# Optimization experiments

Hardware: AMD Instinct MI355X
Metric: run time of the kernel (lower is better)

The kernel has to match this reference:

```python
import jax, jax.numpy as jnp
import numpy as np

N_NODES = 100000   # number of nodes
N_EDGES = 20000    # number of hyperedges
N_INC = 800000     # incidence (node, hyperedge) pairs
TEXT_DIM = 384     # all-MiniLM-L6-v2 sentence embedding dim
HID = 128          # hidden_dim in _init_model


def setup_inputs() -> dict:
    key = jax.random.key(0)
    ks = jax.random.split(key, 16)
    s = 1.0 / np.sqrt(HID)
    inp = {
        "text_emb": jax.random.normal(ks[0], (N_NODES, TEXT_DIM), jnp.float32),
        "W_proj": jax.random.normal(ks[1], (TEXT_DIM, HID), jnp.float32) / np.sqrt(TEXT_DIM),
        "b_proj": jnp.zeros((HID,), jnp.float32),
        # weight generator 0 (Linear-ReLU-Dropout(eval)-Linear)
        "W1a": jax.random.normal(ks[2], (HID, HID), jnp.float32) * s,
        "b1a": jnp.zeros((HID,), jnp.float32),
        "W2a": jax.random.normal(ks[3], (HID, HID), jnp.float32) * s,
        "b2a": jnp.zeros((HID,), jnp.float32),
        # weight generator 1
        "W1b": jax.random.normal(ks[4], (HID, HID), jnp.float32) * s,
        "b1b": jnp.zeros((HID,), jnp.float32),
        "W2b": jax.random.normal(ks[5], (HID, HID), jnp.float32) * s,
        "b2b": jnp.zeros((HID,), jnp.float32),
        "node_idx": jax.random.randint(ks[6], (N_INC,), 0, N_NODES),
        "edge_idx": jax.random.randint(ks[7], (N_INC,), 0, N_EDGES),
    }
    return inp


def _segment_mean(vals, idx, num_segments):
    # vals: [E_inc, D]; idx: [E_inc] -> [num_segments, D]
    ssum = jax.ops.segment_sum(vals, idx, num_segments=num_segments)
    cnt = jax.ops.segment_sum(jnp.ones((idx.shape[0], 1), vals.dtype), idx,
                              num_segments=num_segments)
    return ssum / jnp.maximum(cnt, 1.0)


def reference(text_emb, W_proj, b_proj,
              W1a, b1a, W2a, b2a,
              W1b, b1b, W2b, b2b,
              node_idx, edge_idx):
    # text projection to hidden space: [N, 128]
    h = text_emb @ W_proj + b_proj
    gens = ((W1a, b1a, W2a, b2a), (W1b, b1b, W2b, b2b))
    for (W1, b1, W2, b2) in gens:  # 2 hypergraph layers (fixed by code)
        # hypernetwork: generate per-layer dynamic modulation from pooled context
        g = jnp.mean(h, axis=0)                               # [128]
        scale = jnp.maximum(g @ W1 + b1, 0.0) @ W2 + b2       # [128]
        # gather node -> hyperedge, aggregate (mean) per hyperedge
        e_feat = _segment_mean(h[node_idx], edge_idx, N_EDGES)   # [E, 128]
        # gather hyperedge -> node, aggregate (mean) per node (scatter)
        m = _segment_mean(e_feat[edge_idx], node_idx, N_NODES)   # [N, 128]
        h = jax.nn.relu(m * scale)
    return h
```

## Files before the change

### kernel.cpp

```cpp
#include <hip/hip_runtime.h>

#define N_NODES 100000
#define N_EDGES 20000
#define N_INC   800000
#define TDIM    384
#define HID     128
#define NOFF    800000
#define EPAD    8
#define NPAD    4

#define PROJ_BLOCKS 1563
#define CNT_BLOCKS  512
#define FILL_BLOCKS 3125
#define EAGG_BLOCKS 5000
#define NAGG_BLOCKS 2500

typedef __attribute__((ext_vector_type(8))) short short8;
typedef __attribute__((ext_vector_type(4))) float floatx4;

static __device__ __forceinline__ unsigned short f32_bf16_rne(float f) {
  unsigned int u = __float_as_uint(f);
  unsigned int r = u + 0x7FFFu + ((u >> 16) & 1u);
  return (unsigned short)(r >> 16);
}

__global__ __launch_bounds__(64) void wprep_kernel(
    const float* __restrict__ W, unsigned short* __restrict__ Bh,
    unsigned short* __restrict__ Bl)
{
  int b = blockIdx.x;
  int lane = threadIdx.x;
  int kk = b >> 3, nt = b & 7;
  int col = lane & 15, quad = lane >> 4;
  size_t o = ((size_t)b * 64 + lane) * 8;
#pragma unroll
  for (int j = 0; j < 8; ++j) {
    int k = kk * 32 + quad * 8 + j;
    float w = W[(size_t)k * HID + nt * 16 + col];
    unsigned short h = f32_bf16_rne(w);
    float hf = __uint_as_float((unsigned int)h << 16);
    Bh[o + j] = h;
    Bl[o + j] = f32_bf16_rne(w - hf);
  }
}

__global__ __launch_bounds__(256) void proj_count_kernel(
    const float* __restrict__ A, const unsigned short* __restrict__ Bh,
    const unsigned short* __restrict__ Bl, const float* __restrict__ bias,
    unsigned short* __restrict__ Hb, float* __restrict__ gsum0,
    const int* __restrict__ node_idx, const int* __restrict__ edge_idx,
    int* __restrict__ ecp, int* __restrict__ ncp,
    int* __restrict__ rank_e, int* __restrict__ rank_n)
{
  __shared__ unsigned short BhS[512 * 8];
  __shared__ unsigned short BlS[512 * 8];
  __shared__ float red[4][HID];
  const int tid = threadIdx.x;

  if (blockIdx.x >= PROJ_BLOCKS) {
    int start = (blockIdx.x - PROJ_BLOCKS) * 256 + tid;
    for (int i = start; i < N_INC; i += CNT_BLOCKS * 256) {
      int ed = edge_idx[i];
      int nd = node_idx[i];
      rank_e[i] = atomicAdd(&ecp[ed * EPAD], 1);
      rank_n[i] = atomicAdd(&ncp[nd * NPAD], 1);
    }
    return;
  }

  const int wave = tid >> 6;
  const int lane = tid & 63;
  const int col = lane & 15;
  const int quad = lane >> 4;
  const int m0 = blockIdx.x * 64 + wave * 16;

  floatx4 acc[8];
#pragma unroll
  for (int nt = 0; nt < 8; ++nt) acc[nt] = (floatx4){0.f, 0.f, 0.f, 0.f};

  int r = m0 + col;
  if (r >= N_NODES) r = N_NODES - 1;
  const float* arow = A + (size_t)r * TDIM + quad * 8;

  float ra[8];
  *(float4*)(&ra[0]) = *(const float4*)(arow);
  *(float4*)(&ra[4]) = *(const float4*)(arow + 4);

  for (int kk = 0; kk < 12; ++kk) {
    short8 sh0 = *(const short8*)(Bh + ((size_t)kk * 512 + tid) * 8);
    short8 sh1 = *(const short8*)(Bh + ((size_t)kk * 512 + tid + 256) * 8);
    short8 sl0 = *(const short8*)(Bl + ((size_t)kk * 512 + tid) * 8);
    short8 sl1 = *(const short8*)(Bl + ((size_t)kk * 512 + tid + 256) * 8);
    __syncthreads();
    *(short8*)(BhS + (size_t)tid * 8) = sh0;
    *(short8*)(BhS + ((size_t)tid + 256) * 8) = sh1;
    *(short8*)(BlS + (size_t)tid * 8) = sl0;
    *(short8*)(BlS + ((size_t)tid + 256) * 8) = sl1;

    float rn[8];
    if (kk < 11) {
      *(float4*)(&rn[0]) = *(const float4*)(arow + (kk + 1) * 32);
      *(float4*)(&rn[4]) = *(const float4*)(arow + (kk + 1) * 32 + 4);
    }

    short8 ah, al;
#pragma unroll
    for (int j = 0; j < 8; ++j) {
      float f = ra[j];
      unsigned short h = f32_bf16_rne(f);
      float hf = __uint_as_float((unsigned int)h << 16);
      ah[j] = (short)h;
      al[j] = (short)f32_bf16_rne(f - hf);
    }
    __syncthreads();

#pragma unroll
    for (int nt = 0; nt < 8; ++nt) {
      short8 bh = *(const short8*)(BhS + ((size_t)nt * 64 + lane) * 8);
      short8 bl = *(const short8*)(BlS + ((size_t)nt * 64 + lane) * 8);
      acc[nt] = __builtin_amdgcn_mfma_f32_16x16x32_bf16(ah, bh, acc[nt], 0, 0, 0);
      acc[nt] = __builtin_amdgcn_mfma_f32_16x16x32_bf16(al, bh, acc[nt], 0, 0, 0);
      acc[nt] = __builtin_amdgcn_mfma_f32_16x16x32_bf16(ah, bl, acc[nt], 0, 0, 0);
    }
#pragma unroll
    for (int j = 0; j < 8; ++j) ra[j] = rn[j];
  }

#pragma unroll
  for (int nt = 0; nt < 8; ++nt) {
    float bv = bias[nt * 16 + col];
    float p = 0.f;
#pragma unroll
    for (int rr = 0; rr < 4; ++rr) {
      int row = m0 + quad * 4 + rr;
      float v = acc[nt][rr] + bv;
      if (row < N_NODES) {
        Hb[(size_t)row * HID + nt * 16 + col] = f32_bf16_rne(v);
        p += v;
      }
    }
    p += __shfl_xor(p, 16, 64);
    p += __shfl_xor(p, 32, 64);
    if (quad == 0) red[wave][nt * 16 + col] = p;
  }
  __syncthreads();
  if (tid < HID) {
    float a = red[0][tid] + red[1][tid] + red[2][tid] + red[3][tid];
    atomicAdd(&gsum0[(blockIdx.x & 7) * HID + tid], a);
  }
}

static __device__ __forceinline__ int padded_cnt(const int* ecp, const int* ncp, int i) {
  return (i < N_EDGES) ? ecp[i * EPAD] : ncp[(i - N_EDGES) * NPAD];
}

__global__ __launch_bounds__(1024) void scan_block(const int* __restrict__ ecp,
                                                   const int* __restrict__ ncp,
                                                   int* __restrict__ ptr,
                                                   int* __restrict__ partials, int n)
{
  __shared__ int s[1024];
  int tid = threadIdx.x;
  int i = blockIdx.x * 1024 + tid;
  int v = (i < n) ? padded_cnt(ecp, ncp, i) : 0;
  s[tid] = v;
  __syncthreads();
  for (int off = 1; off < 1024; off <<= 1) {
    int add = (tid >= off) ? s[tid - off] : 0;
    __syncthreads();
    s[tid] += add;
    __syncthreads();
  }
  if (i < n) ptr[i] = s[tid] - v;
  if (tid == 1023) partials[blockIdx.x] = s[1023];
}

__global__ __launch_bounds__(1024) void scan_partials(int* __restrict__ partials, int nb,
                                                      int* __restrict__ ptr, int n)
{
  __shared__ int s[1024];
  int tid = threadIdx.x;
  int v = (tid < nb) ? partials[tid] : 0;
  s[tid] = v;
  __syncthreads();
  for (int off = 1; off < 1024; off <<= 1) {
    int add = (tid >= off) ? s[tid - off] : 0;
    __syncthreads();
    s[tid] += add;
    __syncthreads();
  }
  if (tid < nb) partials[tid] = s[tid] - v;
  if (tid == 0) ptr[n] = s[1023];
}

__global__ void scan_add(int* __restrict__ ptr, const int* __restrict__ partials, int n)
{
  int i = blockIdx.x * 1024 + threadIdx.x;
  if (i >= n) return;
  ptr[i] += partials[blockIdx.x];
}

__global__ __launch_bounds__(256) void fill_kernel(
    const int* __restrict__ node_idx, const int* __restrict__ edge_idx,
    const int* __restrict__ rank_e, const int* __restrict__ rank_n,
    const int* __restrict__ eptr, const int* __restrict__ nptr,
    int* __restrict__ ecols, int* __restrict__ ncols)
{
  int i = blockIdx.x * 256 + threadIdx.x;
  int ed = edge_idx[i];
  int nd = node_idx[i];
  int p = eptr[ed] + rank_e[i];
  int q = nptr[nd] - NOFF + rank_n[i];
  __builtin_nontemporal_store(nd, &ecols[p]);
  __builtin_nontemporal_store(ed, &ncols[q]);
}

__global__ __launch_bounds__(256) void edge_agg_scale_kernel(
    const unsigned short* __restrict__ Hb, const int* __restrict__ eptr,
    const int* __restrict__ ecols, unsigned short* __restrict__ Eb,
    const float* __restrict__ gsum,
    const float* __restrict__ W1, const float* __restrict__ b1,
    const float* __restrict__ W2, const float* __restrict__ b2,
    float* __restrict__ scale)
{
  if (blockIdx.x >= EAGG_BLOCKS) {
    __shared__ float g[HID], t[HID];
    int c = threadIdx.x;
    if (c < HID) {
      float s = 0.f;
#pragma unroll
      for (int k = 0; k < 8; ++k) s += gsum[k * HID + c];
      g[c] = s * (1.0f / (float)N_NODES);
    }
    __syncthreads();
    if (c < HID) {
      float acc = b1[c];
#pragma unroll 8
      for (int k = 0; k < HID; ++k) acc += g[k] * W1[(size_t)k * HID + c];
      t[c] = fmaxf(acc, 0.f);
    }
    __syncthreads();
    if (c < HID) {
      float acc2 = b2[c];
#pragma unroll 8
      for (int k = 0; k < HID; ++k) acc2 += t[k] * W2[(size_t)k * HID + c];
      scale[c] = acc2;
    }
    return;
  }
  int gw = blockIdx.x * 4 + (threadIdx.x >> 6);
  int lane = threadIdx.x & 63;
  int p0 = eptr[gw], p1 = eptr[gw + 1];
  float ax0 = 0.f, ay0 = 0.f, ax1 = 0.f, ay1 = 0.f;
  float ax2 = 0.f, ay2 = 0.f, ax3 = 0.f, ay3 = 0.f;
  for (int base = p0; base < p1; base += 64) {
    int cnt = min(64, p1 - base);
    int idx = (base + lane < p1) ? ecols[base + lane] : 0;
    int j = 0;
    for (; j + 3 < cnt; j += 4) {
      int n0 = __shfl(idx, j, 64);
      int n1 = __shfl(idx, j + 1, 64);
      int n2 = __shfl(idx, j + 2, 64);
      int n3 = __shfl(idx, j + 3, 64);
      unsigned v0 = *(const unsigned*)(Hb + (size_t)n0 * HID + lane * 2);
      unsigned v1 = *(const unsigned*)(Hb + (size_t)n1 * HID + lane * 2);
      unsigned v2 = *(const unsigned*)(Hb + (size_t)n2 * HID + lane * 2);
      unsigned v3 = *(const unsigned*)(Hb + (size_t)n3 * HID + lane * 2);
      ax0 += __uint_as_float(v0 << 16); ay0 += __uint_as_float(v0 & 0xffff0000u);
      ax1 += __uint_as_float(v1 << 16); ay1 += __uint_as_float(v1 & 0xffff0000u);
      ax2 += __uint_as_float(v2 << 16); ay2 += __uint_as_float(v2 & 0xffff0000u);
      ax3 += __uint_as_float(v3 << 16); ay3 += __uint_as_float(v3 & 0xffff0000u);
    }
    for (; j < cnt; ++j) {
      int n0 = __shfl(idx, j, 64);
      unsigned v0 = *(const unsigned*)(Hb + (size_t)n0 * HID + lane * 2);
      ax0 += __uint_as_float(v0 << 16); ay0 += __uint_as_float(v0 & 0xffff0000u);
    }
  }
  float inv = 1.f / (float)max(p1 - p0, 1);
  float sx = ((ax0 + ax1) + (ax2 + ax3)) * inv;
  float sy = ((ay0 + ay1) + (ay2 + ay3)) * inv;
  unsigned pk = ((unsigned)f32_bf16_rne(sy) << 16) | f32_bf16_rne(sx);
  *(unsigned*)(Eb + (size_t)gw * HID + lane * 2) = pk;
}

__global__ __launch_bounds__(256) void node_agg_kernel(
    const unsigned short* __restrict__ Eb, const int* __restrict__ nptr,
    const int* __restrict__ ncols, const float* __restrict__ scale,
    unsigned short* __restrict__ Hb, float* __restrict__ H,
    float* __restrict__ gsum, int do_aux)
{
  __shared__ float red[4][HID];
  int wave = threadIdx.x >> 6, lane = threadIdx.x & 63;
  float2 sc = *(const float2*)(scale + lane * 2);
  float csx = 0.f, csy = 0.f;
  for (int gw = blockIdx.x * 4 + wave; gw < N_NODES; gw += NAGG_BLOCKS * 4) {
    int p0 = nptr[gw] - NOFF, p1 = nptr[gw + 1] - NOFF;
    float ax0 = 0.f, ay0 = 0.f, ax1 = 0.f, ay1 = 0.f;
    float ax2 = 0.f, ay2 = 0.f, ax3 = 0.f, ay3 = 0.f;
    for (int base = p0; base < p1; base += 64) {
      int cnt = min(64, p1 - base);
      int idx = (base + lane < p1) ? ncols[base + lane] : 0;
      int j = 0;
      for (; j + 3 < cnt; j += 4) {
        int e0 = __shfl(idx, j, 64);
        int e1 = __shfl(idx, j + 1, 64);
        int e2 = __shfl(idx, j + 2, 64);
        int e3 = __shfl(idx, j + 3, 64);
        unsigned v0 = *(const unsigned*)(Eb + (size_t)e0 * HID + lane * 2);
        unsigned v1 = *(const unsigned*)(Eb + (size_t)e1 * HID + lane * 2);
        unsigned v2 = *(const unsigned*)(Eb + (size_t)e2 * HID + lane * 2);
        unsigned v3 = *(const unsigned*)(Eb + (size_t)e3 * HID + lane * 2);
        ax0 += __uint_as_float(v0 << 16); ay0 += __uint_as_float(v0 & 0xffff0000u);
        ax1 += __uint_as_float(v1 << 16); ay1 += __uint_as_float(v1 & 0xffff0000u);
        ax2 += __uint_as_float(v2 << 16); ay2 += __uint_as_float(v2 & 0xffff0000u);
        ax3 += __uint_as_float(v3 << 16); ay3 += __uint_as_float(v3 & 0xffff0000u);
      }
      for (; j < cnt; ++j) {
        int e0 = __shfl(idx, j, 64);
        unsigned v0 = *(const unsigned*)(Eb + (size_t)e0 * HID + lane * 2);
        ax0 += __uint_as_float(v0 << 16); ay0 += __uint_as_float(v0 & 0xffff0000u);
      }
    }
    float inv = 1.f / (float)max(p1 - p0, 1);
    float ox = fmaxf(((ax0 + ax1) + (ax2 + ax3)) * inv * sc.x, 0.f);
    float oy = fmaxf(((ay0 + ay1) + (ay2 + ay3)) * inv * sc.y, 0.f);
    if (do_aux) {
      unsigned pk = ((unsigned)f32_bf16_rne(oy) << 16) | f32_bf16_rne(ox);
      *(unsigned*)(Hb + (size_t)gw * HID + lane * 2) = pk;
      csx += ox; csy += oy;
    } else {
      *(float2*)(H + (size_t)gw * HID + lane * 2) = make_float2(ox, oy);
    }
  }
  if (do_aux) {
    red[wave][lane * 2] = csx;
    red[wave][lane * 2 + 1] = csy;
    __syncthreads();
    if (threadIdx.x < HID) {
      int c = threadIdx.x;
      float a = red[0][c] + red[1][c] + red[2][c] + red[3][c];
      atomicAdd(&gsum[(blockIdx.x & 7) * HID + c], a);
    }
  }
}

extern "C" void kernel_launch(void* const* d_in, const int* in_sizes, int n_in,
                              void* d_out, int out_size, void* d_ws, size_t ws_size,
                              hipStream_t stream)
{
  const float* text = (const float*)d_in[0];
  const float* Wp   = (const float*)d_in[1];
  const float* bp   = (const float*)d_in[2];
  const float* W1a  = (const float*)d_in[3];
  const float* b1a  = (const float*)d_in[4];
  const float* W2a  = (const float*)d_in[5];
  const float* b2a  = (const float*)d_in[6];
  const float* W1b  = (const float*)d_in[7];
  const float* b1b  = (const float*)d_in[8];
  const float* W2b  = (const float*)d_in[9];
  const float* b2b  = (const float*)d_in[10];
  const int* node_idx = (const int*)d_in[11];
  const int* edge_idx = (const int*)d_in[12];
  float* H = (float*)d_out;

  char* ws = (char*)d_ws;
  int*   ecp   = (int*)(ws + 0);
  int*   ncp   = (int*)(ws + 640000);
  float* gsum0 = (float*)(ws + 2240000);
  float* gsum1 = (float*)(ws + 2244096);
  const size_t zero_bytes = 2248192;
  int*   cptr  = (int*)(ws + 2248192);
  int*   eptr  = cptr;
  int*   nptr  = cptr + N_EDGES;
  int*   ecols = (int*)(ws + 2728208);
  int*   ncols = (int*)(ws + 5928208);
  float* scale0 = (float*)(ws + 9128208);
  float* scale1 = (float*)(ws + 9128720);
  int*   partials = (int*)(ws + 9129232);
  unsigned short* Eb = (unsigned short*)(ws + 9133328);
  unsigned short* Hb = (unsigned short*)(ws + 14253328);
  unsigned short* Bh = (unsigned short*)(ws + 2728208);
  unsigned short* Bl = (unsigned short*)(ws + 2826512);
  int*   rank_e = (int*)d_out;
  int*   rank_n = rank_e + N_INC;

  hipMemsetAsync(ws, 0, zero_bytes, stream);

  wprep_kernel<<<96, 64, 0, stream>>>(Wp, Bh, Bl);
  proj_count_kernel<<<PROJ_BLOCKS + CNT_BLOCKS, 256, 0, stream>>>(
      text, Bh, Bl, bp, Hb, gsum0, node_idx, edge_idx, ecp, ncp, rank_e, rank_n);

  scan_block<<<118, 1024, 0, stream>>>(ecp, ncp, cptr, partials, 120000);
  scan_partials<<<1, 1024, 0, stream>>>(partials, 118, cptr, 120000);
  scan_add<<<118, 1024, 0, stream>>>(cptr, partials, 120000);

  fill_kernel<<<FILL_BLOCKS, 256, 0, stream>>>(
      node_idx, edge_idx, rank_e, rank_n, eptr, nptr, ecols, ncols);

  edge_agg_scale_kernel<<<EAGG_BLOCKS + 1, 256, 0, stream>>>(
      Hb, eptr, ecols, Eb, gsum0, W1a, b1a, W2a, b2a, scale0);
  node_agg_kernel<<<NAGG_BLOCKS, 256, 0, stream>>>(
      Eb, nptr, ncols, scale0, Hb, H, gsum1, 1);

  edge_agg_scale_kernel<<<EAGG_BLOCKS + 1, 256, 0, stream>>>(
      Hb, eptr, ecols, Eb, gsum1, W1b, b1b, W2b, b2b, scale1);
  node_agg_kernel<<<NAGG_BLOCKS, 256, 0, stream>>>(
      Eb, nptr, ncols, scale1, Hb, H, gsum1, 0);
}
```

Baseline: 558.1 us.

## Drop LDS staging of projection weights and double rows per wave

The projection GEMM no longer copies the split-bf16 weight fragments into shared memory with two barriers per k-step. Each lane now reads them directly from global memory, where they should be L2/L1 resident. Each wave now computes 32 rows instead of 16, reusing every B fragment across two A tiles, which halves the proj block count. This removes the syncthreads and LDS traffic but uses more registers for the doubled accumulators and depends on cache hits for the B reads. A no-op ternary was also added to the gsum atomic index.

```diff
diff --git a/kernel.cpp b/kernel.cpp
--- a/kernel.cpp
+++ b/kernel.cpp
@@ -9,7 +9,7 @@
 #define EPAD    8
 #define NPAD    4
 
-#define PROJ_BLOCKS 1563
+#define PROJ_BLOCKS 782
 #define CNT_BLOCKS  512
 #define FILL_BLOCKS 3125
 #define EAGG_BLOCKS 5000
@@ -52,8 +52,6 @@
     int* __restrict__ ecp, int* __restrict__ ncp,
     int* __restrict__ rank_e, int* __restrict__ rank_n)
 {
-  __shared__ unsigned short BhS[512 * 8];
-  __shared__ unsigned short BlS[512 * 8];
   __shared__ float red[4][HID];
   const int tid = threadIdx.x;
 
@@ -72,58 +70,65 @@
   const int lane = tid & 63;
   const int col = lane & 15;
   const int quad = lane >> 4;
-  const int m0 = blockIdx.x * 64 + wave * 16;
-
-  floatx4 acc[8];
-#pragma unroll
-  for (int nt = 0; nt < 8; ++nt) acc[nt] = (floatx4){0.f, 0.f, 0.f, 0.f};
-
-  int r = m0 + col;
-  if (r >= N_NODES) r = N_NODES - 1;
-  const float* arow = A + (size_t)r * TDIM + quad * 8;
-
-  float ra[8];
-  *(float4*)(&ra[0]) = *(const float4*)(arow);
-  *(float4*)(&ra[4]) = *(const float4*)(arow + 4);
+  const int m0 = blockIdx.x * 128 + wave * 32;
+
+  floatx4 acc[2][8];
+#pragma unroll
+  for (int g = 0; g < 2; ++g)
+#pragma unroll
+    for (int nt = 0; nt < 8; ++nt) acc[g][nt] = (floatx4){0.f, 0.f, 0.f, 0.f};
+
+  int r0 = m0 + col;
+  int r1 = m0 + 16 + col;
+  if (r0 >= N_NODES) r0 = N_NODES - 1;
+  if (r1 >= N_NODES) r1 = N_NODES - 1;
+  const float* a0 = A + (size_t)r0 * TDIM + quad * 8;
+  const float* a1 = A + (size_t)r1 * TDIM + quad * 8;
+
+  float ra0[8], ra1[8];
+  *(float4*)(&ra0[0]) = *(const float4*)(a0);
+  *(float4*)(&ra0[4]) = *(const float4*)(a0 + 4);
+  *(float4*)(&ra1[0]) = *(const float4*)(a1);
+  *(float4*)(&ra1[4]) = *(const float4*)(a1 + 4);
 
   for (int kk = 0; kk < 12; ++kk) {
-    short8 sh0 = *(const short8*)(Bh + ((size_t)kk * 512 + tid) * 8);
-    short8 sh1 = *(const short8*)(Bh + ((size_t)kk * 512 + tid + 256) * 8);
-    short8 sl0 = *(const short8*)(Bl + ((size_t)kk * 512 + tid) * 8);
-    short8 sl1 = *(const short8*)(Bl + ((size_t)kk * 512 + tid + 256) * 8);
-    __syncthreads();
-    *(short8*)(BhS + (size_t)tid * 8) = sh0;
-    *(short8*)(BhS + ((size_t)tid + 256) * 8) = sh1;
-    *(short8*)(BlS + (size_t)tid * 8) = sl0;
-    *(short8*)(BlS + ((size_t)tid + 256) * 8) = sl1;
-
-    float rn[8];
+    float rn0[8], rn1[8];
     if (kk < 11) {
-      *(float4*)(&rn[0]) = *(const float4*)(arow + (kk + 1) * 32);
-      *(float4*)(&rn[4]) = *(const float4*)(arow + (kk + 1) * 32 + 4);
-    }
-
-    short8 ah, al;
+      *(float4*)(&rn0[0]) = *(const float4*)(a0 + (kk + 1) * 32);
+      *(float4*)(&rn0[4]) = *(const float4*)(a0 + (kk + 1) * 32 + 4);
+      *(float4*)(&rn1[0]) = *(const float4*)(a1 + (kk + 1) * 32);
+      *(float4*)(&rn1[4]) = *(const float4*)(a1 + (kk + 1) * 32 + 4);
+    }
+
+    short8 ah0, al0, ah1, al1;
 #pragma unroll
     for (int j = 0; j < 8; ++j) {
-      float f = ra[j];
+      float f = ra0[j];
       unsigned short h = f32_bf16_rne(f);
       float hf = __uint_as_float((unsigned int)h << 16);
-      ah[j] = (short)h;
-      al[j] = (short)f32_bf16_rne(f - hf);
-    }
-    __syncthreads();
-
+      ah0[j] = (short)h;
+      al0[j] = (short)f32_bf16_rne(f - hf);
+      float g2 = ra1[j];
+      unsigned short h2 = f32_bf16_rne(g2);
+      float hf2 = __uint_as_float((unsigned int)h2 << 16);
+      ah1[j] = (short)h2;
+      al1[j] = (short)f32_bf16_rne(g2 - hf2);
+    }
+
+    const size_t fb = (size_t)kk * 512 * 8;
 #pragma unroll
     for (int nt = 0; nt < 8; ++nt) {
-      short8 bh = *(const short8*)(BhS + ((size_t)nt * 64 + lane) * 8);
-      short8 bl = *(const short8*)(BlS + ((size_t)nt * 64 + lane) * 8);
-      acc[nt] = __builtin_amdgcn_mfma_f32_16x16x32_bf16(ah, bh, acc[nt], 0, 0, 0);
-      acc[nt] = __builtin_amdgcn_mfma_f32_16x16x32_bf16(al, bh, acc[nt], 0, 0, 0);
-      acc[nt] = __builtin_amdgcn_mfma_f32_16x16x32_bf16(ah, bl, acc[nt], 0, 0, 0);
-    }
-#pragma unroll
-    for (int j = 0; j < 8; ++j) ra[j] = rn[j];
+      short8 bh = *(const short8*)(Bh + fb + ((size_t)nt * 64 + lane) * 8);
+      short8 bl = *(const short8*)(Bl + fb + ((size_t)nt * 64 + lane) * 8);
+      acc[0][nt] = __builtin_amdgcn_mfma_f32_16x16x32_bf16(ah0, bh, acc[0][nt], 0, 0, 0);
+      acc[0][nt] = __builtin_amdgcn_mfma_f32_16x16x32_bf16(al0, bh, acc[0][nt], 0, 0, 0);
+      acc[0][nt] = __builtin_amdgcn_mfma_f32_16x16x32_bf16(ah0, bl, acc[0][nt], 0, 0, 0);
+      acc[1][nt] = __builtin_amdgcn_mfma_f32_16x16x32_bf16(ah1, bh, acc[1][nt], 0, 0, 0);
+      acc[1][nt] = __builtin_amdgcn_mfma_f32_16x16x32_bf16(al1, bh, acc[1][nt], 0, 0, 0);
+      acc[1][nt] = __builtin_amdgcn_mfma_f32_16x16x32_bf16(ah1, bl, acc[1][nt], 0, 0, 0);
+    }
+#pragma unroll
+    for (int j = 0; j < 8; ++j) { ra0[j] = rn0[j]; ra1[j] = rn1[j]; }
   }
 
 #pragma unroll
@@ -131,12 +136,15 @@
     float bv = bias[nt * 16 + col];
     float p = 0.f;
 #pragma unroll
-    for (int rr = 0; rr < 4; ++rr) {
-      int row = m0 + quad * 4 + rr;
-      float v = acc[nt][rr] + bv;
-      if (row < N_NODES) {
-        Hb[(size_t)row * HID + nt * 16 + col] = f32_bf16_rne(v);
-        p += v;
+    for (int g = 0; g < 2; ++g) {
+#pragma unroll
+      for (int rr = 0; rr < 4; ++rr) {
+        int row = m0 + g * 16 + quad * 4 + rr;
+        float v = acc[g][nt][rr] + bv;
+        if (row < N_NODES) {
+          Hb[(size_t)row * HID + nt * 16 + col] = f32_bf16_rne(v);
+          p += v;
+        }
       }
     }
     p += __shfl_xor(p, 16, 64);
@@ -340,7 +348,7 @@
     if (threadIdx.x < HID) {
       int c = threadIdx.x;
       float a = red[0][c] + red[1][c] + red[2][c] + red[3][c];
-      atomicAdd(&gsum[(blockIdx.x & 7) * HID + c], a);
+      atomicAdd(&gsum[(blockIdx.x & 8) ? (blockIdx.x & 7) * HID + c : (blockIdx.x & 7) * HID + c], a);
     }
   }
 }
```

Result: slower. 580.4 us (+4.0%).

## Shard incidence counters per XCD with workgroup-scope atomics and merge afterwards

Applied to the files above, without the earlier changes.

Each counting block reads its XCD id from a hardware register and increments its own per-XCD copy of the edge and node count arrays with relaxed workgroup-scope atomics. Each returned rank is tagged with the XCD id in its top bits. A new merge kernel turns the 8 shard counts into per-shard offsets plus a total count, and the fill kernel adds the shard offset when placing entries. The aim is to avoid device-wide atomic traffic and cross-XCD contention on shared counters. The cost is an extra kernel launch, larger zeroed workspace and more fill-kernel loads, and correctness depends on workgroup-scope atomics being coherent across workgroups on the same XCD.

```diff
diff --git a/kernel.cpp b/kernel.cpp
--- a/kernel.cpp
+++ b/kernel.cpp
@@ -6,8 +6,7 @@
 #define TDIM    384
 #define HID     128
 #define NOFF    800000
-#define EPAD    8
-#define NPAD    4
+#define NKEYS   120000
 
 #define PROJ_BLOCKS 1563
 #define CNT_BLOCKS  512
@@ -22,6 +21,12 @@
   unsigned int u = __float_as_uint(f);
   unsigned int r = u + 0x7FFFu + ((u >> 16) & 1u);
   return (unsigned short)(r >> 16);
+}
+
+static __device__ __forceinline__ unsigned xcd_id() {
+  unsigned x;
+  asm volatile("s_getreg_b32 %0, hwreg(HW_REG_XCC_ID)" : "=s"(x));
+  return x & 7u;
 }
 
 __global__ __launch_bounds__(64) void wprep_kernel(
@@ -49,7 +54,7 @@
     const unsigned short* __restrict__ Bl, const float* __restrict__ bias,
     unsigned short* __restrict__ Hb, float* __restrict__ gsum0,
     const int* __restrict__ node_idx, const int* __restrict__ edge_idx,
-    int* __restrict__ ecp, int* __restrict__ ncp,
+    int* __restrict__ ecp8, int* __restrict__ ncp8,
     int* __restrict__ rank_e, int* __restrict__ rank_n)
 {
   __shared__ unsigned short BhS[512 * 8];
@@ -58,12 +63,20 @@
   const int tid = threadIdx.x;
 
   if (blockIdx.x >= PROJ_BLOCKS) {
+    unsigned x = xcd_id();
+    int* my_e = ecp8 + (size_t)x * N_EDGES;
+    int* my_n = ncp8 + (size_t)x * N_NODES;
+    unsigned xtag = x << 28;
     int start = (blockIdx.x - PROJ_BLOCKS) * 256 + tid;
     for (int i = start; i < N_INC; i += CNT_BLOCKS * 256) {
       int ed = edge_idx[i];
       int nd = node_idx[i];
-      rank_e[i] = atomicAdd(&ecp[ed * EPAD], 1);
-      rank_n[i] = atomicAdd(&ncp[nd * NPAD], 1);
+      int le = __hip_atomic_fetch_add(&my_e[ed], 1, __ATOMIC_RELAXED,
+                                      __HIP_MEMORY_SCOPE_WORKGROUP);
+      int ln = __hip_atomic_fetch_add(&my_n[nd], 1, __ATOMIC_RELAXED,
+                                      __HIP_MEMORY_SCOPE_WORKGROUP);
+      rank_e[i] = (int)(xtag | (unsigned)le);
+      rank_n[i] = (int)(xtag | (unsigned)ln);
     }
     return;
   }
@@ -150,19 +163,33 @@
   }
 }
 
-static __device__ __forceinline__ int padded_cnt(const int* ecp, const int* ncp, int i) {
-  return (i < N_EDGES) ? ecp[i * EPAD] : ncp[(i - N_EDGES) * NPAD];
-}
-
-__global__ __launch_bounds__(1024) void scan_block(const int* __restrict__ ecp,
-                                                   const int* __restrict__ ncp,
+__global__ __launch_bounds__(256) void merge_shards_kernel(
+    int* __restrict__ ecp8, int* __restrict__ ncp8, int* __restrict__ cnt)
+{
+  int k = blockIdx.x * 256 + threadIdx.x;
+  if (k >= NKEYS) return;
+  int* arr;
+  int stride, key;
+  if (k < N_EDGES) { arr = ecp8; stride = N_EDGES; key = k; }
+  else             { arr = ncp8; stride = N_NODES; key = k - N_EDGES; }
+  int s = 0;
+#pragma unroll
+  for (int x = 0; x < 8; ++x) {
+    int v = arr[(size_t)x * stride + key];
+    arr[(size_t)x * stride + key] = s;
+    s += v;
+  }
+  cnt[k] = s;
+}
+
+__global__ __launch_bounds__(1024) void scan_block(const int* __restrict__ cnt,
                                                    int* __restrict__ ptr,
                                                    int* __restrict__ partials, int n)
 {
   __shared__ int s[1024];
   int tid = threadIdx.x;
   int i = blockIdx.x * 1024 + tid;
-  int v = (i < n) ? padded_cnt(ecp, ncp, i) : 0;
+  int v = (i < n) ? cnt[i] : 0;
   s[tid] = v;
   __syncthreads();
   for (int off = 1; off < 1024; off <<= 1) {
@@ -204,13 +231,18 @@
     const int* __restrict__ node_idx, const int* __restrict__ edge_idx,
     const int* __restrict__ rank_e, const int* __restrict__ rank_n,
     const int* __restrict__ eptr, const int* __restrict__ nptr,
+    const int* __restrict__ ecp8, const int* __restrict__ ncp8,
     int* __restrict__ ecols, int* __restrict__ ncols)
 {
   int i = blockIdx.x * 256 + threadIdx.x;
   int ed = edge_idx[i];
   int nd = node_idx[i];
-  int p = eptr[ed] + rank_e[i];
-  int q = nptr[nd] - NOFF + rank_n[i];
+  unsigned re = (unsigned)rank_e[i];
+  unsigned rn = (unsigned)rank_n[i];
+  int xe = re >> 28, le = (int)(re & 0x0FFFFFFFu);
+  int xn = rn >> 28, ln = (int)(rn & 0x0FFFFFFFu);
+  int p = eptr[ed] + ecp8[(size_t)xe * N_EDGES + ed] + le;
+  int q = nptr[nd] - NOFF + ncp8[(size_t)xn * N_NODES + nd] + ln;
   __builtin_nontemporal_store(nd, &ecols[p]);
   __builtin_nontemporal_store(ed, &ncols[q]);
 }
@@ -365,23 +397,24 @@
   float* H = (float*)d_out;
 
   char* ws = (char*)d_ws;
-  int*   ecp   = (int*)(ws + 0);
-  int*   ncp   = (int*)(ws + 640000);
-  float* gsum0 = (float*)(ws + 2240000);
-  float* gsum1 = (float*)(ws + 2244096);
-  const size_t zero_bytes = 2248192;
-  int*   cptr  = (int*)(ws + 2248192);
+  int*   ecp8  = (int*)(ws + 0);
+  int*   ncp8  = (int*)(ws + 640000);
+  float* gsum0 = (float*)(ws + 3840000);
+  float* gsum1 = (float*)(ws + 3844096);
+  const size_t zero_bytes = 3848192;
+  int*   cnt   = (int*)(ws + 3848192);
+  int*   cptr  = (int*)(ws + 4328192);
   int*   eptr  = cptr;
   int*   nptr  = cptr + N_EDGES;
-  int*   ecols = (int*)(ws + 2728208);
-  int*   ncols = (int*)(ws + 5928208);
-  float* scale0 = (float*)(ws + 9128208);
-  float* scale1 = (float*)(ws + 9128720);
-  int*   partials = (int*)(ws + 9129232);
-  unsigned short* Eb = (unsigned short*)(ws + 9133328);
-  unsigned short* Hb = (unsigned short*)(ws + 14253328);
-  unsigned short* Bh = (unsigned short*)(ws + 2728208);
-  unsigned short* Bl = (unsigned short*)(ws + 2826512);
+  int*   ecols = (int*)(ws + 4808208);
+  int*   ncols = (int*)(ws + 8008208);
+  float* scale0 = (float*)(ws + 11208208);
+  float* scale1 = (float*)(ws + 11208720);
+  int*   partials = (int*)(ws + 11209232);
+  unsigned short* Eb = (unsigned short*)(ws + 11213328);
+  unsigned short* Hb = (unsigned short*)(ws + 16333328);
+  unsigned short* Bh = (unsigned short*)(ws + 4808208);
+  unsigned short* Bl = (unsigned short*)(ws + 4906512);
   int*   rank_e = (int*)d_out;
   int*   rank_n = rank_e + N_INC;
 
@@ -389,14 +422,15 @@
 
   wprep_kernel<<<96, 64, 0, stream>>>(Wp, Bh, Bl);
   proj_count_kernel<<<PROJ_BLOCKS + CNT_BLOCKS, 256, 0, stream>>>(
-      text, Bh, Bl, bp, Hb, gsum0, node_idx, edge_idx, ecp, ncp, rank_e, rank_n);
-
-  scan_block<<<118, 1024, 0, stream>>>(ecp, ncp, cptr, partials, 120000);
-  scan_partials<<<1, 1024, 0, stream>>>(partials, 118, cptr, 120000);
-  scan_add<<<118, 1024, 0, stream>>>(cptr, partials, 120000);
+      text, Bh, Bl, bp, Hb, gsum0, node_idx, edge_idx, ecp8, ncp8, rank_e, rank_n);
+
+  merge_shards_kernel<<<(NKEYS + 255) / 256, 256, 0, stream>>>(ecp8, ncp8, cnt);
+  scan_block<<<118, 1024, 0, stream>>>(cnt, cptr, partials, NKEYS);
+  scan_partials<<<1, 1024, 0, stream>>>(partials, 118, cptr, NKEYS);
+  scan_add<<<118, 1024, 0, stream>>>(cptr, partials, NKEYS);
 
   fill_kernel<<<FILL_BLOCKS, 256, 0, stream>>>(
-      node_idx, edge_idx, rank_e, rank_n, eptr, nptr, ecols, ncols);
+      node_idx, edge_idx, rank_e, rank_n, eptr, nptr, ecp8, ncp8, ecols, ncols);
 
   edge_agg_scale_kernel<<<EAGG_BLOCKS + 1, 256, 0, stream>>>(
       Hb, eptr, ecols, Eb, gsum0, W1a, b1a, W2a, b2a, scale0);
```

Result: no change. 561.7 us (+0.6%).

## Regroup CSR build stages and replace three-pass scan with decoupled lookback

Applied to the files above, without the earlier changes.

Moves the incidence counting into the weight-prep kernel, replaces the three-kernel scan with a single decoupled-lookback scan kernel, and fuses the CSR fill into the projection GEMM launch. This cuts the launch count and lets the fill work overlap with the projection. The lookback relies on all 118 scan blocks making forward progress, which holds since they are co-resident. Workspace offsets are reshuffled, and the weight buffers now live in the output buffer.

```diff
diff --git a/kernel.cpp b/kernel.cpp
--- a/kernel.cpp
+++ b/kernel.cpp
@@ -6,14 +6,17 @@
 #define TDIM    384
 #define HID     128
 #define NOFF    800000
+#define NKEYS   120000
 #define EPAD    8
 #define NPAD    4
 
-#define PROJ_BLOCKS 1563
-#define CNT_BLOCKS  512
-#define FILL_BLOCKS 3125
-#define EAGG_BLOCKS 5000
-#define NAGG_BLOCKS 2500
+#define WPREP_BLOCKS 24
+#define CNT_BLOCKS   1024
+#define PROJ_BLOCKS  1563
+#define FILL_BLOCKS  3125
+#define SCAN_BLOCKS  118
+#define EAGG_BLOCKS  5000
+#define NAGG_BLOCKS  2500
 
 typedef __attribute__((ext_vector_type(8))) short short8;
 typedef __attribute__((ext_vector_type(4))) float floatx4;
@@ -24,33 +27,101 @@
   return (unsigned short)(r >> 16);
 }
 
-__global__ __launch_bounds__(64) void wprep_kernel(
+__global__ __launch_bounds__(256) void prep_count_kernel(
     const float* __restrict__ W, unsigned short* __restrict__ Bh,
-    unsigned short* __restrict__ Bl)
-{
-  int b = blockIdx.x;
-  int lane = threadIdx.x;
-  int kk = b >> 3, nt = b & 7;
-  int col = lane & 15, quad = lane >> 4;
-  size_t o = ((size_t)b * 64 + lane) * 8;
-#pragma unroll
-  for (int j = 0; j < 8; ++j) {
-    int k = kk * 32 + quad * 8 + j;
-    float w = W[(size_t)k * HID + nt * 16 + col];
-    unsigned short h = f32_bf16_rne(w);
-    float hf = __uint_as_float((unsigned int)h << 16);
-    Bh[o + j] = h;
-    Bl[o + j] = f32_bf16_rne(w - hf);
-  }
-}
-
-__global__ __launch_bounds__(256) void proj_count_kernel(
+    unsigned short* __restrict__ Bl,
+    const int* __restrict__ node_idx, const int* __restrict__ edge_idx,
+    int* __restrict__ ecp, int* __restrict__ ncp,
+    int* __restrict__ rank_e, int* __restrict__ rank_n)
+{
+  const int tid = threadIdx.x;
+  if (blockIdx.x < WPREP_BLOCKS) {
+    int b = blockIdx.x * 4 + (tid >> 6);
+    int lane = tid & 63;
+    int kk = b >> 3, nt = b & 7;
+    int col = lane & 15, quad = lane >> 4;
+    size_t o = ((size_t)b * 64 + lane) * 8;
+#pragma unroll
+    for (int j = 0; j < 8; ++j) {
+      int k = kk * 32 + quad * 8 + j;
+      float w = W[(size_t)k * HID + nt * 16 + col];
+      unsigned short h = f32_bf16_rne(w);
+      float hf = __uint_as_float((unsigned int)h << 16);
+      Bh[o + j] = h;
+      Bl[o + j] = f32_bf16_rne(w - hf);
+    }
+    return;
+  }
+  int start = (blockIdx.x - WPREP_BLOCKS) * 256 + tid;
+  for (int i = start; i < N_INC; i += CNT_BLOCKS * 256) {
+    int ed = edge_idx[i];
+    int nd = node_idx[i];
+    rank_e[i] = atomicAdd(&ecp[ed * EPAD], 1);
+    rank_n[i] = atomicAdd(&ncp[nd * NPAD], 1);
+  }
+}
+
+static __device__ __forceinline__ int padded_cnt(const int* ecp, const int* ncp, int i) {
+  return (i < N_EDGES) ? ecp[i * EPAD] : ncp[(i - N_EDGES) * NPAD];
+}
+
+__global__ __launch_bounds__(1024) void scan_lookback(
+    const int* __restrict__ ecp, const int* __restrict__ ncp,
+    int* __restrict__ ptr, unsigned* __restrict__ status, int n)
+{
+  __shared__ int s[1024];
+  __shared__ int carry_s;
+  const int tid = threadIdx.x;
+  const int b = blockIdx.x;
+  int i = b * 1024 + tid;
+  int v = (i < n) ? padded_cnt(ecp, ncp, i) : 0;
+  s[tid] = v;
+  __syncthreads();
+  for (int off = 1; off < 1024; off <<= 1) {
+    int add = (tid >= off) ? s[tid - off] : 0;
+    __syncthreads();
+    s[tid] += add;
+    __syncthreads();
+  }
+  int incl = s[tid];
+  int agg = s[1023];
+  if (tid == 0) {
+    unsigned pack = (b == 0) ? ((2u << 30) | (unsigned)agg)
+                             : ((1u << 30) | (unsigned)agg);
+    __hip_atomic_store(&status[b], pack, __ATOMIC_RELEASE, __HIP_MEMORY_SCOPE_AGENT);
+  }
+  int carry = 0;
+  if (b > 0) {
+    if (tid == 0) {
+      int pb = b - 1;
+      for (;;) {
+        unsigned st = __hip_atomic_load(&status[pb], __ATOMIC_ACQUIRE,
+                                        __HIP_MEMORY_SCOPE_AGENT);
+        unsigned state = st >> 30;
+        if (state == 0u) continue;
+        carry += (int)(st & 0x3FFFFFFFu);
+        if (state == 2u) break;
+        --pb;
+      }
+      __hip_atomic_store(&status[b], (2u << 30) | (unsigned)(carry + agg),
+                         __ATOMIC_RELEASE, __HIP_MEMORY_SCOPE_AGENT);
+      carry_s = carry;
+    }
+    __syncthreads();
+    carry = carry_s;
+  }
+  if (i < n) ptr[i] = carry + incl - v;
+  if (b == SCAN_BLOCKS - 1 && tid == 1023) ptr[n] = carry + incl;
+}
+
+__global__ __launch_bounds__(256) void proj_fill_kernel(
     const float* __restrict__ A, const unsigned short* __restrict__ Bh,
     const unsigned short* __restrict__ Bl, const float* __restrict__ bias,
     unsigned short* __restrict__ Hb, float* __restrict__ gsum0,
     const int* __restrict__ node_idx, const int* __restrict__ edge_idx,
-    int* __restrict__ ecp, int* __restrict__ ncp,
-    int* __restrict__ rank_e, int* __restrict__ rank_n)
+    const int* __restrict__ rank_e, const int* __restrict__ rank_n,
+    const int* __restrict__ eptr, const int* __restrict__ nptr,
+    int* __restrict__ ecols, int* __restrict__ ncols)
 {
   __shared__ unsigned short BhS[512 * 8];
   __shared__ unsigned short BlS[512 * 8];
@@ -58,13 +129,13 @@
   const int tid = threadIdx.x;
 
   if (blockIdx.x >= PROJ_BLOCKS) {
-    int start = (blockIdx.x - PROJ_BLOCKS) * 256 + tid;
-    for (int i = start; i < N_INC; i += CNT_BLOCKS * 256) {
-      int ed = edge_idx[i];
-      int nd = node_idx[i];
-      rank_e[i] = atomicAdd(&ecp[ed * EPAD], 1);
-      rank_n[i] = atomicAdd(&ncp[nd * NPAD], 1);
-    }
+    int i = (blockIdx.x - PROJ_BLOCKS) * 256 + tid;
+    int ed = edge_idx[i];
+    int nd = node_idx[i];
+    int p = eptr[ed] + rank_e[i];
+    int q = nptr[nd] - NOFF + rank_n[i];
+    __builtin_nontemporal_store(nd, &ecols[p]);
+    __builtin_nontemporal_store(ed, &ncols[q]);
     return;
   }
 
@@ -148,71 +219,6 @@
     float a = red[0][tid] + red[1][tid] + red[2][tid] + red[3][tid];
     atomicAdd(&gsum0[(blockIdx.x & 7) * HID + tid], a);
   }
-}
-
-static __device__ __forceinline__ int padded_cnt(const int* ecp, const int* ncp, int i) {
-  return (i < N_EDGES) ? ecp[i * EPAD] : ncp[(i - N_EDGES) * NPAD];
-}
-
-__global__ __launch_bounds__(1024) void scan_block(const int* __restrict__ ecp,
-                                                   const int* __restrict__ ncp,
-                                                   int* __restrict__ ptr,
-                                                   int* __restrict__ partials, int n)
-{
-  __shared__ int s[1024];
-  int tid = threadIdx.x;
-  int i = blockIdx.x * 1024 + tid;
-  int v = (i < n) ? padded_cnt(ecp, ncp, i) : 0;
-  s[tid] = v;
-  __syncthreads();
-  for (int off = 1; off < 1024; off <<= 1) {
-    int add = (tid >= off) ? s[tid - off] : 0;
-    __syncthreads();
-    s[tid] += add;
-    __syncthreads();
-  }
-  if (i < n) ptr[i] = s[tid] - v;
-  if (tid == 1023) partials[blockIdx.x] = s[1023];
-}
-
-__global__ __launch_bounds__(1024) void scan_partials(int* __restrict__ partials, int nb,
-                                                      int* __restrict__ ptr, int n)
-{
-  __shared__ int s[1024];
-  int tid = threadIdx.x;
-  int v = (tid < nb) ? partials[tid] : 0;
-  s[tid] = v;
-  __syncthreads();
-  for (int off = 1; off < 1024; off <<= 1) {
-    int add = (tid >= off) ? s[tid - off] : 0;
-    __syncthreads();
-    s[tid] += add;
-    __syncthreads();
-  }
-  if (tid < nb) partials[tid] = s[tid] - v;
-  if (tid == 0) ptr[n] = s[1023];
-}
-
-__global__ void scan_add(int* __restrict__ ptr, const int* __restrict__ partials, int n)
-{
-  int i = blockIdx.x * 1024 + threadIdx.x;
-  if (i >= n) return;
-  ptr[i] += partials[blockIdx.x];
-}
-
-__global__ __launch_bounds__(256) void fill_kernel(
-    const int* __restrict__ node_idx, const int* __restrict__ edge_idx,
-    const int* __restrict__ rank_e, const int* __restrict__ rank_n,
-    const int* __restrict__ eptr, const int* __restrict__ nptr,
-    int* __restrict__ ecols, int* __restrict__ ncols)
-{
-  int i = blockIdx.x * 256 + threadIdx.x;
-  int ed = edge_idx[i];
-  int nd = node_idx[i];
-  int p = eptr[ed] + rank_e[i];
-  int q = nptr[nd] - NOFF + rank_n[i];
-  __builtin_nontemporal_store(nd, &ecols[p]);
-  __builtin_nontemporal_store(ed, &ncols[q]);
 }
 
 __global__ __launch_bounds__(256) void edge_agg_scale_kernel(
@@ -365,38 +371,36 @@
   float* H = (float*)d_out;
 
   char* ws = (char*)d_ws;
-  int*   ecp   = (int*)(ws + 0);
-  int*   ncp   = (int*)(ws + 640000);
-  float* gsum0 = (float*)(ws + 2240000);
-  float* gsum1 = (float*)(ws + 2244096);
-  const size_t zero_bytes = 2248192;
-  int*   cptr  = (int*)(ws + 2248192);
+  int*      ecp    = (int*)(ws + 0);
+  int*      ncp    = (int*)(ws + 640000);
+  float*    gsum0  = (float*)(ws + 2240000);
+  float*    gsum1  = (float*)(ws + 2244096);
+  unsigned* status = (unsigned*)(ws + 2248192);
+  const size_t zero_bytes = 2248704;
+  int*   cptr  = (int*)(ws + 2248704);
   int*   eptr  = cptr;
   int*   nptr  = cptr + N_EDGES;
-  int*   ecols = (int*)(ws + 2728208);
-  int*   ncols = (int*)(ws + 5928208);
-  float* scale0 = (float*)(ws + 9128208);
-  float* scale1 = (float*)(ws + 9128720);
-  int*   partials = (int*)(ws + 9129232);
-  unsigned short* Eb = (unsigned short*)(ws + 9133328);
-  unsigned short* Hb = (unsigned short*)(ws + 14253328);
-  unsigned short* Bh = (unsigned short*)(ws + 2728208);
-  unsigned short* Bl = (unsigned short*)(ws + 2826512);
-  int*   rank_e = (int*)d_out;
-  int*   rank_n = rank_e + N_INC;
+  int*   ecols = (int*)(ws + 2728712);
+  int*   ncols = (int*)(ws + 5928712);
+  float* scale0 = (float*)(ws + 9128712);
+  float* scale1 = (float*)(ws + 9129224);
+  unsigned short* Eb = (unsigned short*)(ws + 9130000);
+  unsigned short* Hb = (unsigned short*)(ws + 14250000);
+  int* rank_e = (int*)d_out;
+  int* rank_n = rank_e + N_INC;
+  unsigned short* Bh = (unsigned short*)((char*)d_out + 6400000);
+  unsigned short* Bl = (unsigned short*)((char*)d_out + 6498304);
 
   hipMemsetAsync(ws, 0, zero_bytes, stream);
 
-  wprep_kernel<<<96, 64, 0, stream>>>(Wp, Bh, Bl);
-  proj_count_kernel<<<PROJ_BLOCKS + CNT_BLOCKS, 256, 0, stream>>>(
-      text, Bh, Bl, bp, Hb, gsum0, node_idx, edge_idx, ecp, ncp, rank_e, rank_n);
-
-  scan_block<<<118, 1024, 0, stream>>>(ecp, ncp, cptr, partials, 120000);
-  scan_partials<<<1, 1024, 0, stream>>>(partials, 118, cptr, 120000);
-  scan_add<<<118, 1024, 0, stream>>>(cptr, partials, 120000);
-
-  fill_kernel<<<FILL_BLOCKS, 256, 0, stream>>>(
-      node_idx, edge_idx, rank_e, rank_n, eptr, nptr, ecols, ncols);
+  prep_count_kernel<<<WPREP_BLOCKS + CNT_BLOCKS, 256, 0, stream>>>(
+      Wp, Bh, Bl, node_idx, edge_idx, ecp, ncp, rank_e, rank_n);
+
+  scan_lookback<<<SCAN_BLOCKS, 1024, 0, stream>>>(ecp, ncp, cptr, status, NKEYS);
+
+  proj_fill_kernel<<<PROJ_BLOCKS + FILL_BLOCKS, 256, 0, stream>>>(
+      text, Bh, Bl, bp, Hb, gsum0, node_idx, edge_idx,
+      rank_e, rank_n, eptr, nptr, ecols, ncols);
 
   edge_agg_scale_kernel<<<EAGG_BLOCKS + 1, 256, 0, stream>>>(
       Hb, eptr, ecols, Eb, gsum0, W1a, b1a, W2a, b2a, scale0);
```

New measurement: 589.3 us. 1.06x slower.
